# Kernel tuning notes

Hardware: AMD Instinct MI355X
Metric: run time of the kernel (lower is better)

The kernel has to match this reference:

```python
import math
import jax, jax.numpy as jnp
import numpy as np

NH, NKV, HD, THETA = 32, 8, 128, 500000.0

def rotate_half(x):
    x1, x2 = jnp.split(x, 2, axis=-1)
    return jnp.concatenate((-x2, x1), axis=-1)

def rope_cos_sin(seq_len, dim, base, dtype):
    inv_freq = 1.0 / (base ** (jnp.arange(0, dim, 2, dtype=jnp.float32) / dim))
    t = jnp.arange(seq_len, dtype=jnp.float32)
    freqs = jnp.outer(t, inv_freq)              # [S, dim/2]
    emb = jnp.concatenate((freqs, freqs), -1)   # [S, dim]
    return jnp.cos(emb).astype(dtype), jnp.sin(emb).astype(dtype)

def setup_inputs() -> dict:
    key = jax.random.key(0)
    ks = jax.random.split(key, 5)
    B, S, H = 1, 2048, 4096
    sc = 1.0 / math.sqrt(H)
    return {
        'x':  jax.random.normal(ks[0], (B, S, H), jnp.float32),
        'wq': jax.random.normal(ks[1], (H, H), jnp.float32) * sc,
        'wk': jax.random.normal(ks[2], (NKV * HD, H), jnp.float32) * sc,
        'wv': jax.random.normal(ks[3], (NKV * HD, H), jnp.float32) * sc,
        'wo': jax.random.normal(ks[4], (H, H), jnp.float32) * sc,
    }

def attention(x, wq, wk, wv, wo):
    B, S, H = x.shape
    n_rep = NH // NKV
    q = (x @ wq.T).reshape(B, S, NH, HD).transpose(0, 2, 1, 3)    # [B,NH,S,HD]
    k = (x @ wk.T).reshape(B, S, NKV, HD).transpose(0, 2, 1, 3)   # [B,NKV,S,HD]
    v = (x @ wv.T).reshape(B, S, NKV, HD).transpose(0, 2, 1, 3)
    cos, sin = rope_cos_sin(S, HD, THETA, x.dtype)                # [S,HD]
    cos = cos[None, None]; sin = sin[None, None]
    q = q * cos + rotate_half(q) * sin
    k = k * cos + rotate_half(k) * sin
    k = jnp.repeat(k, n_rep, axis=1)                               # [B,NH,S,HD]
    v = jnp.repeat(v, n_rep, axis=1)
    scores = jnp.einsum('bhqd,bhkd->bhqk', q, k) / math.sqrt(HD)
    causal = jnp.tril(jnp.ones((S, S), dtype=bool))
    scores = jnp.where(causal, scores, jnp.finfo(scores.dtype).min)
    probs = jax.nn.softmax(scores, axis=-1)
    out = jnp.einsum('bhqk,bhkd->bhqd', probs, v)                  # [B,NH,S,HD]
    out = out.transpose(0, 2, 1, 3).reshape(B, S, H)
    return out @ wo.T

def reference(x, wq, wk, wv, wo):
    return attention(x, wq, wk, wv, wo)
```

## Files before the change

### kernel.cpp

```cpp
#include <hip/hip_runtime.h>
#include <hip/hip_bf16.h>
#include <math.h>

typedef __bf16 bf16x8 __attribute__((ext_vector_type(8)));
typedef __bf16 bf16x4 __attribute__((ext_vector_type(4)));
typedef unsigned short u16x8 __attribute__((ext_vector_type(8)));
typedef float  f32x4  __attribute__((ext_vector_type(4)));

constexpr int kS   = 2048;
constexpr int kH   = 4096;
constexpr int kNH  = 32;
constexpr int kNKV = 8;
constexpr int kHD  = 128;
constexpr int kQKV = kH + 2 * kNKV * kHD;
constexpr int kKOff = kH;
constexpr int kVOff = kH + kNKV * kHD;

__global__ void cast_bf16(const float* __restrict__ in, __bf16* __restrict__ out, int n4) {
    int i = blockIdx.x * blockDim.x + threadIdx.x;
    if (i < n4) {
        float4 f = ((const float4*)in)[i];
        bf16x4 o;
        o[0] = (__bf16)f.x; o[1] = (__bf16)f.y; o[2] = (__bf16)f.z; o[3] = (__bf16)f.w;
        ((bf16x4*)out)[i] = o;
    }
}

__global__ void cast_all(const float* __restrict__ x, const float* __restrict__ wq,
                         const float* __restrict__ wk, const float* __restrict__ wv,
                         __bf16* __restrict__ xb, __bf16* __restrict__ wqkv) {
    int i = blockIdx.x * 256 + threadIdx.x;
    float4 f;
    __bf16* dst;
    int di;
    if (i < (1 << 21)) {
        f = ((const float4*)x)[i];
        dst = xb; di = i;
    } else {
        int j = i - (1 << 21);
        const float4* s = (j < (1 << 22)) ? ((const float4*)wq + j)
                        : (j < (5 << 20)) ? ((const float4*)wk + (j - (1 << 22)))
                                          : ((const float4*)wv + (j - (5 << 20)));
        f = *s;
        dst = wqkv; di = j;
    }
    bf16x4 o;
    o[0] = (__bf16)f.x; o[1] = (__bf16)f.y; o[2] = (__bf16)f.z; o[3] = (__bf16)f.w;
    ((bf16x4*)dst)[di] = o;
}

__device__ inline void gld16(const __bf16* g, __bf16* l) {
    __builtin_amdgcn_global_load_lds((const __attribute__((address_space(1))) void*)g,
                                     (__attribute__((address_space(3))) void*)l, 16, 0, 0);
}

constexpr int GBK = 32, GBM = 128;

template <typename OutT, int GBN>
__global__ __launch_bounds__(512, 2) void gemm8(const __bf16* __restrict__ A,
                                                const __bf16* __restrict__ B,
                                                OutT* __restrict__ C,
                                                int M, int N, int K, int nbx) {
    constexpr int FM  = 4;
    constexpr int FN  = GBN / 64;
    constexpr int AL  = GBM / 128;
    constexpr int BL  = GBN / 128;
    constexpr int GPK = AL + BL;
    constexpr int ASZ = GBM * GBK;
    constexpr int BSZ = GBN * GBK;

    __shared__ __align__(16) __bf16 Ab[4][ASZ];
    __shared__ __align__(16) __bf16 Bb[4][BSZ];

    const int tid = threadIdx.x, w = tid >> 6, lane = tid & 63;
    const int lr = lane & 15, g = lane >> 4;

    const int nwg = (int)gridDim.x;
    const int bid = (int)blockIdx.x;
    int trow, tcol;
    if (nwg == 256 && nbx == 16) {
        const int xcd = bid & 7, j = bid >> 3;
        trow = (xcd >> 1) * 4 + (j >> 3);
        tcol = (xcd & 1) * 8 + (j & 7);
    } else {
        const int id2 = (bid & 7) * (nwg >> 3) + (bid >> 3);
        trow = id2 / nbx; tcol = id2 % nbx;
    }
    const int m0 = trow * GBM, n0 = tcol * GBN;

    const int wm = (w >> 2) * 64, wn = (w & 3) * (GBN / 4);

    const __bf16* ga[AL]; int la[AL];
    const __bf16* gb[BL]; int lb[BL];
#pragma unroll
    for (int a = 0; a < AL; a++) {
        int G = a * 512 + tid, row = G >> 2;
        int lg = (G & 3) ^ ((row >> 1) & 3);
        ga[a] = A + (size_t)(m0 + row) * K + lg * 8;
        la[a] = G * 8;
    }
#pragma unroll
    for (int b = 0; b < BL; b++) {
        int G = b * 512 + tid, row = G >> 2;
        int lg = (G & 3) ^ ((row >> 1) & 3);
        gb[b] = B + (size_t)(n0 + row) * K + lg * 8;
        lb[b] = G * 8;
    }

    int pao[FM], pbo[FN];
    const int sw = (lr >> 1) & 3;
#pragma unroll
    for (int i = 0; i < FM; i++) pao[i] = (wm + i * 16 + lr) * GBK + ((g ^ sw) * 8);
#pragma unroll
    for (int j = 0; j < FN; j++) pbo[j] = (wn + j * 16 + lr) * GBK + ((g ^ sw) * 8);

    f32x4 acc[FM][FN];
#pragma unroll
    for (int i = 0; i < FM; i++)
#pragma unroll
        for (int j = 0; j < FN; j++) acc[i][j] = (f32x4)(0.f);

    const int NT = K / GBK;

#pragma unroll
    for (int z = 0; z < 3; z++) {
#pragma unroll
        for (int a = 0; a < AL; a++) gld16(ga[a] + z * GBK, &Ab[z][la[a]]);
#pragma unroll
        for (int b = 0; b < BL; b++) gld16(gb[b] + z * GBK, &Bb[z][lb[b]]);
    }
    if constexpr (GPK == 4) asm volatile("s_waitcnt vmcnt(8)" ::: "memory");
    else                    asm volatile("s_waitcnt vmcnt(6)" ::: "memory");
    __builtin_amdgcn_s_barrier();

    for (int Z = 0; Z < NT; ++Z) {
        const int q = Z & 3, qs = (Z + 3) & 3;

        bf16x8 af[FM], bfr[FN];
#pragma unroll
        for (int i = 0; i < FM; i++) af[i]  = *(const bf16x8*)&Ab[q][pao[i]];
#pragma unroll
        for (int j = 0; j < FN; j++) bfr[j] = *(const bf16x8*)&Bb[q][pbo[j]];

        if (Z < NT - 3) {
#pragma unroll
            for (int a = 0; a < AL; a++) gld16(ga[a] + (Z + 3) * GBK, &Ab[qs][la[a]]);
#pragma unroll
            for (int b = 0; b < BL; b++) gld16(gb[b] + (Z + 3) * GBK, &Bb[qs][lb[b]]);
        }

        __builtin_amdgcn_s_barrier();
        __builtin_amdgcn_s_setprio(1);
#pragma unroll
        for (int i = 0; i < FM; i++)
#pragma unroll
            for (int j = 0; j < FN; j++)
                acc[i][j] = __builtin_amdgcn_mfma_f32_16x16x32_bf16(
                    af[i], bfr[j], acc[i][j], 0, 0, 0);
        __builtin_amdgcn_s_setprio(0);

        if (Z < NT - 3) {
            if constexpr (GPK == 4) asm volatile("s_waitcnt vmcnt(8)" ::: "memory");
            else                    asm volatile("s_waitcnt vmcnt(6)" ::: "memory");
        } else if (Z == NT - 3) {
            if constexpr (GPK == 4) asm volatile("s_waitcnt vmcnt(4)" ::: "memory");
            else                    asm volatile("s_waitcnt vmcnt(3)" ::: "memory");
        } else if (Z == NT - 2) {
            asm volatile("s_waitcnt vmcnt(0)" ::: "memory");
        }
        __builtin_amdgcn_s_barrier();
    }

    const int cr = g * 4, cc = lr;
#pragma unroll
    for (int i = 0; i < FM; i++)
#pragma unroll
        for (int j = 0; j < FN; j++) {
            OutT* Cp = C + (size_t)(m0 + wm + i * 16 + cr) * N + (n0 + wn + j * 16 + cc);
#pragma unroll
            for (int r = 0; r < 4; r++) Cp[(size_t)r * N] = (OutT)acc[i][j][r];
        }
}

__global__ void rope_qkv(__bf16* __restrict__ qkv) {
    int idx  = blockIdx.x * 256 + threadIdx.x;
    int d8   = idx & 7;
    int rest = idx >> 3;
    int hh   = rest % (kNH + kNKV);
    int s    = rest / (kNH + kNKV);
    __bf16* base = qkv + (size_t)s * kQKV + ((hh < kNH) ? hh * kHD : kKOff + (hh - kNH) * kHD);
    float sc = (hh < kNH) ? 0.088388347648318447f : 1.0f;
    bf16x8 va = *(const bf16x8*)(base + d8 * 8);
    bf16x8 vb = *(const bf16x8*)(base + 64 + d8 * 8);
    bf16x8 ra, rb;
#pragma unroll
    for (int j = 0; j < 8; j++) {
        int d = d8 * 8 + j;
        float rev = (float)s * exp2f(fmaf((float)d, -0.2958057589f, -2.6514961295f));
        rev -= floorf(rev);
        float ang = rev * 6.28318530718f;
        float sn = __sinf(ang), cs = __cosf(ang);
        float a = (float)va[j], b = (float)vb[j];
        ra[j] = (__bf16)((a * cs - b * sn) * sc);
        rb[j] = (__bf16)((b * cs + a * sn) * sc);
    }
    *(bf16x8*)(base + d8 * 8)      = ra;
    *(bf16x8*)(base + 64 + d8 * 8) = rb;
}

constexpr int VTP = 72;

__global__ __launch_bounds__(256) void flash_attn(const __bf16* __restrict__ qkv,
                                                  __bf16* __restrict__ ob) {
    __shared__ __align__(16) __bf16 Ks[2][64 * 128];
    __shared__ __align__(16) __bf16 Vt[2][128 * VTP];
    __shared__ __align__(16) __bf16 Ps[4 * 16 * 64];

    const int tid  = threadIdx.x;
    const int wave = tid >> 6, lane = tid & 63;
    const int bx   = blockIdx.x;
    const int kvh  = bx & 7;
    const int qt   = 127 - (bx >> 3);
    const int h    = kvh * 4 + wave;
    const int r    = lane & 15, g = lane >> 4;
    const int r7   = r & 7;
    const int qglob = qt * 16 + r;

    __bf16* Pw = Ps + wave * 16 * 64;
    const __bf16* kbase = qkv + kKOff + kvh * kHD;
    const __bf16* vbase = qkv + kVOff + kvh * kHD;

    int krow[4], kgc[4];
#pragma unroll
    for (int c = 0; c < 4; c++) {
        krow[c] = wave * 16 + c * 4 + (lane >> 4);
        kgc[c]  = (lane & 15) ^ (krow[c] & 15);
    }
    int vp[2], vc[2];
#pragma unroll
    for (int i = 0; i < 2; i++) {
        int task = i * 256 + tid;
        vp[i] = task & 31; vc[i] = task >> 5;
    }

    bf16x8 qfrag[4];
    const __bf16* qrow = qkv + (size_t)(qt * 16 + r) * kQKV + h * kHD + g * 8;
#pragma unroll
    for (int c = 0; c < 4; c++) qfrag[c] = *(const bf16x8*)(qrow + c * 32);

    f32x4 o[8];
#pragma unroll
    for (int dt = 0; dt < 8; dt++) o[dt] = (f32x4)(0.f);
    float mrow = -3.0e38f, lrow = 0.f;

    const int nkt = qt / 4 + 1;

    bf16x8 va[2], vb[2];
#pragma unroll
    for (int c = 0; c < 4; c++)
        gld16(kbase + (size_t)krow[c] * kQKV + kgc[c] * 8, &Ks[0][(wave * 4 + c) * 512]);
#pragma unroll
    for (int i = 0; i < 2; i++) {
        const __bf16* v0 = vbase + (size_t)(2 * vp[i]) * kQKV + vc[i] * 8;
        va[i] = *(const bf16x8*)v0;
        vb[i] = *(const bf16x8*)(v0 + kQKV);
    }
    asm volatile("s_waitcnt vmcnt(0)" ::: "memory");
#pragma unroll
    for (int i = 0; i < 2; i++) {
        u16x8 a = __builtin_bit_cast(u16x8, va[i]);
        u16x8 b = __builtin_bit_cast(u16x8, vb[i]);
#pragma unroll
        for (int j = 0; j < 8; j++) {
            unsigned int pk = (unsigned int)a[j] | ((unsigned int)b[j] << 16);
            *(unsigned int*)(&Vt[0][(vc[i] * 8 + j) * VTP + 2 * vp[i]]) = pk;
        }
    }
    __syncthreads();

    for (int kt = 0; kt < nkt; ++kt) {
        const int cur = kt & 1, nb = cur ^ 1;
        const bool nxt = (kt + 1) < nkt;

        if (nxt) {
#pragma unroll
            for (int c = 0; c < 4; c++)
                gld16(kbase + (size_t)((kt + 1) * 64 + krow[c]) * kQKV + kgc[c] * 8,
                      &Ks[nb][(wave * 4 + c) * 512]);
#pragma unroll
            for (int i = 0; i < 2; i++) {
                const __bf16* v0 = vbase + (size_t)((kt + 1) * 64 + 2 * vp[i]) * kQKV + vc[i] * 8;
                va[i] = *(const bf16x8*)v0;
                vb[i] = *(const bf16x8*)(v0 + kQKV);
            }
        }

        f32x4 st[4];
#pragma unroll
        for (int t = 0; t < 4; t++) st[t] = (f32x4)(0.f);
#pragma unroll
        for (int c = 0; c < 4; c++) {
#pragma unroll
            for (int t = 0; t < 4; t++) {
                bf16x8 kf = *(const bf16x8*)&Ks[cur][(t * 16 + r) * 128 + (((c * 4 + g) ^ r) * 8)];
                st[t] = __builtin_amdgcn_mfma_f32_16x16x32_bf16(kf, qfrag[c], st[t], 0, 0, 0);
            }
        }

        if (kt == nkt - 1) {
#pragma unroll
            for (int t = 0; t < 4; t++)
#pragma unroll
                for (int reg = 0; reg < 4; reg++) {
                    int key = kt * 64 + t * 16 + g * 4 + reg;
                    if (key > qglob) st[t][reg] = -3.0e38f;
                }
        }

        float mloc = -3.0e38f;
#pragma unroll
        for (int t = 0; t < 4; t++)
#pragma unroll
            for (int reg = 0; reg < 4; reg++) mloc = fmaxf(mloc, st[t][reg]);
        mloc = fmaxf(mloc, __shfl_xor(mloc, 16));
        mloc = fmaxf(mloc, __shfl_xor(mloc, 32));
        float mnew  = fmaxf(mrow, mloc);
        float alpha = __expf(mrow - mnew);
        mrow = mnew;
        float lsum = 0.f;
#pragma unroll
        for (int t = 0; t < 4; t++)
#pragma unroll
            for (int reg = 0; reg < 4; reg++) {
                float pv = __expf(st[t][reg] - mnew);
                st[t][reg] = pv;
                lsum += pv;
            }
        lsum += __shfl_xor(lsum, 16);
        lsum += __shfl_xor(lsum, 32);
        lrow = lrow * alpha + lsum;

        float ar[4];
#pragma unroll
        for (int reg = 0; reg < 4; reg++) ar[reg] = __shfl(alpha, g * 4 + reg);
#pragma unroll
        for (int dt = 0; dt < 8; dt++)
#pragma unroll
            for (int reg = 0; reg < 4; reg++) o[dt][reg] *= ar[reg];

        if (nxt) {
            asm volatile("s_waitcnt vmcnt(0)" ::: "memory");
#pragma unroll
            for (int i = 0; i < 2; i++) {
                u16x8 a = __builtin_bit_cast(u16x8, va[i]);
                u16x8 b = __builtin_bit_cast(u16x8, vb[i]);
#pragma unroll
                for (int j = 0; j < 8; j++) {
                    unsigned int pk = (unsigned int)a[j] | ((unsigned int)b[j] << 16);
                    *(unsigned int*)(&Vt[nb][(vc[i] * 8 + j) * VTP + 2 * vp[i]]) = pk;
                }
            }
        }

#pragma unroll
        for (int t = 0; t < 4; t++) {
            bf16x4 pb;
#pragma unroll
            for (int j = 0; j < 4; j++) pb[j] = (__bf16)st[t][j];
            int p8 = t * 4 + g;
            *(bf16x4*)&Pw[r * 64 + (((p8 >> 1) ^ r7) * 8) + ((p8 & 1) * 4)] = pb;
        }
        __asm__ volatile("s_waitcnt lgkmcnt(0)" ::: "memory");

#pragma unroll
        for (int kc = 0; kc < 2; kc++) {
            bf16x8 pf = *(const bf16x8*)&Pw[r * 64 + (((kc * 4 + g) ^ r7) * 8)];
#pragma unroll
            for (int dt = 0; dt < 8; dt++) {
                bf16x8 vf = *(const bf16x8*)&Vt[cur][(dt * 16 + r) * VTP + kc * 32 + g * 8];
                o[dt] = __builtin_amdgcn_mfma_f32_16x16x32_bf16(pf, vf, o[dt], 0, 0, 0);
            }
        }
        __syncthreads();
    }

    float linv = 1.f / lrow;
    float lr4[4];
#pragma unroll
    for (int reg = 0; reg < 4; reg++) lr4[reg] = __shfl(linv, g * 4 + reg);
#pragma unroll
    for (int dt = 0; dt < 8; dt++)
#pragma unroll
        for (int reg = 0; reg < 4; reg++) {
            int qq = g * 4 + reg, dd = dt * 16 + r;
            ob[(size_t)(qt * 16 + qq) * kH + h * kHD + dd] = (__bf16)(o[dt][reg] * lr4[reg]);
        }
}

extern "C" void kernel_launch(void* const* d_in, const int* in_sizes, int n_in,
                              void* d_out, int out_size, void* d_ws, size_t ws_size,
                              hipStream_t stream) {
    const float* x  = (const float*)d_in[0];
    const float* wq = (const float*)d_in[1];
    const float* wk = (const float*)d_in[2];
    const float* wv = (const float*)d_in[3];
    const float* wo = (const float*)d_in[4];
    float* out = (float*)d_out;

    char* p = (char*)d_ws;
    auto alloc = [&](size_t bytes) {
        char* r = p;
        p += (bytes + 255) & ~(size_t)255;
        return r;
    };
    __bf16* xb    = (__bf16*)alloc((size_t)kS * kH * 2);
    __bf16* wqkvb = (__bf16*)alloc((size_t)kQKV * kH * 2);
    __bf16* qkv   = (__bf16*)alloc((size_t)kS * kQKV * 2);
    __bf16* ao    = xb;
    __bf16* wob   = wqkvb;

    cast_all<<<dim3(1 << 15), 256, 0, stream>>>(x, wq, wk, wv, xb, wqkvb);

    gemm8<__bf16, 384><<<dim3((kS / GBM) * (kQKV / 384)), 512, 0, stream>>>(
        xb, wqkvb, qkv, kS, kQKV, kH, kQKV / 384);

    rope_qkv<<<dim3(kS * (kNH + kNKV) * 8 / 256), 256, 0, stream>>>(qkv);

    cast_bf16<<<dim3((kH * kH / 4) / 256), 256, 0, stream>>>(wo, wob, kH * kH / 4);

    flash_attn<<<dim3(kNKV * (kS / 16)), 256, 0, stream>>>(qkv, ao);

    gemm8<float, 256><<<dim3((kS / GBM) * (kH / 256)), 512, 0, stream>>>(
        ao, wob, out, kS, kH, kH, kH / 256);
}
```

Before: 472.1 us.

## Add 256x256 ping-pong GEMM for QKV projection and fuse wo cast

Replaces the QKV projection GEMM with a new 256x256-tile kernel. It double-buffers LDS with a 64-wide K step and splits each K step into four quadrant phases, interleaving async global-to-LDS loads with MFMA work and raising wave priority around the MFMA blocks. The wo fp32-to-bf16 cast moves into the single cast_all launch, which drops one kernel launch and now needs a separate wob buffer instead of reusing wqkvb. Priority hints are also added around the MFMA loops in flash attention. The larger tiles raise register and LDS pressure, and the grid has only 192 workgroups, which may underfill the GPU.

```diff
diff --git a/kernel.cpp b/kernel.cpp
--- a/kernel.cpp
+++ b/kernel.cpp
@@ -16,19 +16,11 @@
 constexpr int kKOff = kH;
 constexpr int kVOff = kH + kNKV * kHD;
 
-__global__ void cast_bf16(const float* __restrict__ in, __bf16* __restrict__ out, int n4) {
-    int i = blockIdx.x * blockDim.x + threadIdx.x;
-    if (i < n4) {
-        float4 f = ((const float4*)in)[i];
-        bf16x4 o;
-        o[0] = (__bf16)f.x; o[1] = (__bf16)f.y; o[2] = (__bf16)f.z; o[3] = (__bf16)f.w;
-        ((bf16x4*)out)[i] = o;
-    }
-}
-
 __global__ void cast_all(const float* __restrict__ x, const float* __restrict__ wq,
                          const float* __restrict__ wk, const float* __restrict__ wv,
-                         __bf16* __restrict__ xb, __bf16* __restrict__ wqkv) {
+                         const float* __restrict__ wo,
+                         __bf16* __restrict__ xb, __bf16* __restrict__ wqkv,
+                         __bf16* __restrict__ wob) {
     int i = blockIdx.x * 256 + threadIdx.x;
     float4 f;
     __bf16* dst;
@@ -38,11 +30,17 @@
         dst = xb; di = i;
     } else {
         int j = i - (1 << 21);
-        const float4* s = (j < (1 << 22)) ? ((const float4*)wq + j)
-                        : (j < (5 << 20)) ? ((const float4*)wk + (j - (1 << 22)))
-                                          : ((const float4*)wv + (j - (5 << 20)));
-        f = *s;
-        dst = wqkv; di = j;
+        if (j < (6 << 20)) {
+            const float4* s = (j < (1 << 22)) ? ((const float4*)wq + j)
+                            : (j < (5 << 20)) ? ((const float4*)wk + (j - (1 << 22)))
+                                              : ((const float4*)wv + (j - (5 << 20)));
+            f = *s;
+            dst = wqkv; di = j;
+        } else {
+            int k = j - (6 << 20);
+            f = ((const float4*)wo)[k];
+            dst = wob; di = k;
+        }
     }
     bf16x4 o;
     o[0] = (__bf16)f.x; o[1] = (__bf16)f.y; o[2] = (__bf16)f.z; o[3] = (__bf16)f.w;
@@ -52,6 +50,122 @@
 __device__ inline void gld16(const __bf16* g, __bf16* l) {
     __builtin_amdgcn_global_load_lds((const __attribute__((address_space(1))) void*)g,
                                      (__attribute__((address_space(3))) void*)l, 16, 0, 0);
+}
+
+constexpr int TBK = 64;
+
+__global__ __launch_bounds__(512, 2) void gemm256(const __bf16* __restrict__ A,
+                                                  const __bf16* __restrict__ B,
+                                                  __bf16* __restrict__ C,
+                                                  int M, int N, int K, int nbx) {
+    __shared__ __align__(16) __bf16 Ab[2][256 * TBK];
+    __shared__ __align__(16) __bf16 Bb[2][256 * TBK];
+
+    const int tid = threadIdx.x, w = tid >> 6, lane = tid & 63;
+    const int lr = lane & 15, g4 = lane >> 4, s7 = lane & 7;
+
+    const int nwg = (int)gridDim.x, bid = (int)blockIdx.x;
+    const int id2 = (bid & 7) * (nwg >> 3) + (bid >> 3);
+    const int m0 = (id2 / nbx) * 256, n0 = (id2 % nbx) * 256;
+
+    const int wmq = (w >> 2) * 64;
+    const int wnq = (w & 3) * 32;
+
+    const int srow = tid >> 3;
+    const int slg  = (tid & 7) ^ (srow & 7);
+    const __bf16* gA = A + (size_t)(m0 + srow) * K + slg * 8;
+    const __bf16* gB = B + (size_t)(n0 + srow) * K + slg * 8;
+
+    int pk[2];
+#pragma unroll
+    for (int kc = 0; kc < 2; kc++) pk[kc] = (((kc * 4 + g4) ^ s7) * 8);
+
+    bf16x8 a[4][2], b[2][2];
+    f32x4 acc[8][4];
+#pragma unroll
+    for (int i = 0; i < 8; i++)
+#pragma unroll
+        for (int j = 0; j < 4; j++) acc[i][j] = (f32x4)(0.f);
+
+    const int NT = K / TBK;
+
+#define STAGE_A(h, kt, bf) { _Pragma("unroll") for (int e = 0; e < 2; e++) \
+    gld16(gA + (size_t)((h) * 128 + e * 64) * K + (kt) * TBK, \
+          &Ab[bf][(h) * 8192 + (e * 512 + tid) * 8]); }
+#define STAGE_B(h, kt, bf) { _Pragma("unroll") for (int e = 0; e < 2; e++) \
+    gld16(gB + (size_t)((h) * 128 + e * 64) * K + (kt) * TBK, \
+          &Bb[bf][(h) * 8192 + (e * 512 + tid) * 8]); }
+#define DSA(qi) { _Pragma("unroll") for (int i = 0; i < 4; i++) { \
+    const int ro = ((qi) * 128 + wmq + i * 16 + lr) * TBK; \
+    a[i][0] = *(const bf16x8*)&Ab[q][ro + pk[0]]; \
+    a[i][1] = *(const bf16x8*)&Ab[q][ro + pk[1]]; } }
+#define DSB(qj) { _Pragma("unroll") for (int j = 0; j < 2; j++) { \
+    const int ro = ((qj) * 128 + wnq + j * 16 + lr) * TBK; \
+    b[j][0] = *(const bf16x8*)&Bb[q][ro + pk[0]]; \
+    b[j][1] = *(const bf16x8*)&Bb[q][ro + pk[1]]; } }
+#define MMA(qi, qj) { _Pragma("unroll") for (int kc = 0; kc < 2; kc++) \
+    _Pragma("unroll") for (int i = 0; i < 4; i++) \
+    _Pragma("unroll") for (int j = 0; j < 2; j++) \
+        acc[(qi) * 4 + i][(qj) * 2 + j] = __builtin_amdgcn_mfma_f32_16x16x32_bf16( \
+            a[i][kc], b[j][kc], acc[(qi) * 4 + i][(qj) * 2 + j], 0, 0, 0); }
+#define LGKM0 asm volatile("s_waitcnt lgkmcnt(0)" ::: "memory")
+#define VM(n) asm volatile("s_waitcnt vmcnt(" #n ")" ::: "memory")
+#define BAR __builtin_amdgcn_s_barrier()
+#define PRIO(x) __builtin_amdgcn_s_setprio(x)
+
+    STAGE_A(0, 0, 0); STAGE_B(0, 0, 0); STAGE_A(1, 0, 0); STAGE_B(1, 0, 0);
+    VM(4);
+    BAR;
+
+    for (int Z = 0; Z < NT; ++Z) {
+        const int q = Z & 1, nb = q ^ 1;
+        const bool stg = Z < NT - 1;
+
+        DSA(0); DSB(0);
+        if (stg) STAGE_A(0, Z + 1, nb);
+        BAR; LGKM0;
+        PRIO(1); MMA(0, 0); PRIO(0);
+        if (stg) { VM(4); } else { VM(2); }
+        BAR;
+
+        DSA(1);
+        if (stg) STAGE_B(0, Z + 1, nb);
+        BAR; LGKM0;
+        PRIO(1); MMA(1, 0); PRIO(0);
+        if (stg) { VM(4); } else { VM(0); }
+        BAR;
+
+        DSB(1);
+        if (stg) STAGE_A(1, Z + 1, nb);
+        BAR; LGKM0;
+        PRIO(1); MMA(1, 1); PRIO(0);
+        BAR;
+
+        DSA(0);
+        if (stg) STAGE_B(1, Z + 1, nb);
+        BAR; LGKM0;
+        PRIO(1); MMA(0, 1); PRIO(0);
+        if (stg) { VM(4); }
+        BAR;
+    }
+
+#undef STAGE_A
+#undef STAGE_B
+#undef DSA
+#undef DSB
+#undef MMA
+
+    const int cr = g4 * 4, cc = lr;
+#pragma unroll
+    for (int fi = 0; fi < 8; fi++)
+#pragma unroll
+        for (int fj = 0; fj < 4; fj++) {
+            const int row = m0 + (fi >> 2) * 128 + wmq + (fi & 3) * 16 + cr;
+            const int col = n0 + (fj >> 1) * 128 + wnq + (fj & 1) * 16 + cc;
+            __bf16* Cp = C + (size_t)row * N + col;
+#pragma unroll
+            for (int r = 0; r < 4; r++) Cp[(size_t)r * N] = (__bf16)acc[fi][fj][r];
+        }
 }
 
 constexpr int GBK = 32, GBM = 128;
@@ -298,6 +412,7 @@
         f32x4 st[4];
 #pragma unroll
         for (int t = 0; t < 4; t++) st[t] = (f32x4)(0.f);
+        __builtin_amdgcn_s_setprio(1);
 #pragma unroll
         for (int c = 0; c < 4; c++) {
 #pragma unroll
@@ -306,6 +421,7 @@
                 st[t] = __builtin_amdgcn_mfma_f32_16x16x32_bf16(kf, qfrag[c], st[t], 0, 0, 0);
             }
         }
+        __builtin_amdgcn_s_setprio(0);
 
         if (kt == nkt - 1) {
 #pragma unroll
@@ -372,6 +488,7 @@
         }
         __asm__ volatile("s_waitcnt lgkmcnt(0)" ::: "memory");
 
+        __builtin_amdgcn_s_setprio(1);
 #pragma unroll
         for (int kc = 0; kc < 2; kc++) {
             bf16x8 pf = *(const bf16x8*)&Pw[r * 64 + (((kc * 4 + g) ^ r7) * 8)];
@@ -381,6 +498,7 @@
                 o[dt] = __builtin_amdgcn_mfma_f32_16x16x32_bf16(pf, vf, o[dt], 0, 0, 0);
             }
         }
+        __builtin_amdgcn_s_setprio(0);
         __syncthreads();
     }
 
@@ -416,17 +534,15 @@
     __bf16* xb    = (__bf16*)alloc((size_t)kS * kH * 2);
     __bf16* wqkvb = (__bf16*)alloc((size_t)kQKV * kH * 2);
     __bf16* qkv   = (__bf16*)alloc((size_t)kS * kQKV * 2);
+    __bf16* wob   = (__bf16*)alloc((size_t)kH * kH * 2);
     __bf16* ao    = xb;
-    __bf16* wob   = wqkvb;
-
-    cast_all<<<dim3(1 << 15), 256, 0, stream>>>(x, wq, wk, wv, xb, wqkvb);
-
-    gemm8<__bf16, 384><<<dim3((kS / GBM) * (kQKV / 384)), 512, 0, stream>>>(
-        xb, wqkvb, qkv, kS, kQKV, kH, kQKV / 384);
+
+    cast_all<<<dim3(49152), 256, 0, stream>>>(x, wq, wk, wv, wo, xb, wqkvb, wob);
+
+    gemm256<<<dim3((kS / 256) * (kQKV / 256)), 512, 0, stream>>>(
+        xb, wqkvb, qkv, kS, kQKV, kH, kQKV / 256);
 
     rope_qkv<<<dim3(kS * (kNH + kNKV) * 8 / 256), 256, 0, stream>>>(qkv);
-
-    cast_bf16<<<dim3((kH * kH / 4) / 256), 256, 0, stream>>>(wo, wob, kH * kH / 4);
 
     flash_attn<<<dim3(kNKV * (kS / 16)), 256, 0, stream>>>(qkv, ao);
 
```

Result: slower. 522.2 us (+10.6%).

## Process two query tiles per wave in flash attention and fold wo cast into cast_all

Applied to the files above, without the earlier changes.

Each flash-attention wave now handles two 16-row query fragments (32 queries per block), so every K/V tile loaded into LDS feeds twice as many MFMAs and the grid is halved. The K/V double buffering is removed in favour of single-buffered loads with a synchronous wait, with launch_bounds(256,2) and s_setprio raised around the MFMA sections. Query tiles are ordered to interleave long and short causal rows for balance. The wo weight cast is merged into the single cast_all launch with its own workspace buffer, dropping a separate kernel launch. The cost is that load latency is no longer overlapped within a block and more registers are used.

```diff
diff --git a/kernel.cpp b/kernel.cpp
--- a/kernel.cpp
+++ b/kernel.cpp
@@ -16,19 +16,11 @@
 constexpr int kKOff = kH;
 constexpr int kVOff = kH + kNKV * kHD;
 
-__global__ void cast_bf16(const float* __restrict__ in, __bf16* __restrict__ out, int n4) {
-    int i = blockIdx.x * blockDim.x + threadIdx.x;
-    if (i < n4) {
-        float4 f = ((const float4*)in)[i];
-        bf16x4 o;
-        o[0] = (__bf16)f.x; o[1] = (__bf16)f.y; o[2] = (__bf16)f.z; o[3] = (__bf16)f.w;
-        ((bf16x4*)out)[i] = o;
-    }
-}
-
 __global__ void cast_all(const float* __restrict__ x, const float* __restrict__ wq,
                          const float* __restrict__ wk, const float* __restrict__ wv,
-                         __bf16* __restrict__ xb, __bf16* __restrict__ wqkv) {
+                         const float* __restrict__ wo,
+                         __bf16* __restrict__ xb, __bf16* __restrict__ wqkv,
+                         __bf16* __restrict__ wob) {
     int i = blockIdx.x * 256 + threadIdx.x;
     float4 f;
     __bf16* dst;
@@ -38,11 +30,17 @@
         dst = xb; di = i;
     } else {
         int j = i - (1 << 21);
-        const float4* s = (j < (1 << 22)) ? ((const float4*)wq + j)
-                        : (j < (5 << 20)) ? ((const float4*)wk + (j - (1 << 22)))
-                                          : ((const float4*)wv + (j - (5 << 20)));
-        f = *s;
-        dst = wqkv; di = j;
+        if (j < (6 << 20)) {
+            const float4* s = (j < (1 << 22)) ? ((const float4*)wq + j)
+                            : (j < (5 << 20)) ? ((const float4*)wk + (j - (1 << 22)))
+                                              : ((const float4*)wv + (j - (5 << 20)));
+            f = *s;
+            dst = wqkv; di = j;
+        } else {
+            int k = j - (6 << 20);
+            f = ((const float4*)wo)[k];
+            dst = wob; di = k;
+        }
     }
     bf16x4 o;
     o[0] = (__bf16)f.x; o[1] = (__bf16)f.y; o[2] = (__bf16)f.z; o[3] = (__bf16)f.w;
@@ -210,23 +208,22 @@
 
 constexpr int VTP = 72;
 
-__global__ __launch_bounds__(256) void flash_attn(const __bf16* __restrict__ qkv,
-                                                  __bf16* __restrict__ ob) {
-    __shared__ __align__(16) __bf16 Ks[2][64 * 128];
-    __shared__ __align__(16) __bf16 Vt[2][128 * VTP];
-    __shared__ __align__(16) __bf16 Ps[4 * 16 * 64];
+__global__ __launch_bounds__(256, 2) void flash_attn(const __bf16* __restrict__ qkv,
+                                                     __bf16* __restrict__ ob) {
+    __shared__ __align__(16) __bf16 Ks[64 * 128];
+    __shared__ __align__(16) __bf16 Vt[128 * VTP];
+    __shared__ __align__(16) __bf16 Ps[8 * 16 * 64];
 
     const int tid  = threadIdx.x;
     const int wave = tid >> 6, lane = tid & 63;
     const int bx   = blockIdx.x;
     const int kvh  = bx & 7;
-    const int qt   = 127 - (bx >> 3);
+    const int p    = bx >> 3;
+    const int qt2  = (p < 32) ? (63 - p) : (p - 32);
     const int h    = kvh * 4 + wave;
     const int r    = lane & 15, g = lane >> 4;
     const int r7   = r & 7;
-    const int qglob = qt * 16 + r;
-
-    __bf16* Pw = Ps + wave * 16 * 64;
+
     const __bf16* kbase = qkv + kKOff + kvh * kHD;
     const __bf16* vbase = qkv + kVOff + kvh * kHD;
 
@@ -243,158 +240,154 @@
         vp[i] = task & 31; vc[i] = task >> 5;
     }
 
-    bf16x8 qfrag[4];
-    const __bf16* qrow = qkv + (size_t)(qt * 16 + r) * kQKV + h * kHD + g * 8;
-#pragma unroll
-    for (int c = 0; c < 4; c++) qfrag[c] = *(const bf16x8*)(qrow + c * 32);
-
-    f32x4 o[8];
-#pragma unroll
-    for (int dt = 0; dt < 8; dt++) o[dt] = (f32x4)(0.f);
-    float mrow = -3.0e38f, lrow = 0.f;
-
-    const int nkt = qt / 4 + 1;
-
-    bf16x8 va[2], vb[2];
-#pragma unroll
-    for (int c = 0; c < 4; c++)
-        gld16(kbase + (size_t)krow[c] * kQKV + kgc[c] * 8, &Ks[0][(wave * 4 + c) * 512]);
-#pragma unroll
-    for (int i = 0; i < 2; i++) {
-        const __bf16* v0 = vbase + (size_t)(2 * vp[i]) * kQKV + vc[i] * 8;
-        va[i] = *(const bf16x8*)v0;
-        vb[i] = *(const bf16x8*)(v0 + kQKV);
-    }
-    asm volatile("s_waitcnt vmcnt(0)" ::: "memory");
-#pragma unroll
-    for (int i = 0; i < 2; i++) {
-        u16x8 a = __builtin_bit_cast(u16x8, va[i]);
-        u16x8 b = __builtin_bit_cast(u16x8, vb[i]);
-#pragma unroll
-        for (int j = 0; j < 8; j++) {
-            unsigned int pk = (unsigned int)a[j] | ((unsigned int)b[j] << 16);
-            *(unsigned int*)(&Vt[0][(vc[i] * 8 + j) * VTP + 2 * vp[i]]) = pk;
-        }
-    }
-    __syncthreads();
-
+    bf16x8 qfrag[2][4];
+#pragma unroll
+    for (int f = 0; f < 2; f++) {
+        const __bf16* qrow = qkv + (size_t)(qt2 * 32 + f * 16 + r) * kQKV + h * kHD + g * 8;
+#pragma unroll
+        for (int c = 0; c < 4; c++) qfrag[f][c] = *(const bf16x8*)(qrow + c * 32);
+    }
+
+    f32x4 o[2][8];
+#pragma unroll
+    for (int f = 0; f < 2; f++)
+#pragma unroll
+        for (int dt = 0; dt < 8; dt++) o[f][dt] = (f32x4)(0.f);
+    float mrow[2] = {-3.0e38f, -3.0e38f}, lrow[2] = {0.f, 0.f};
+
+    const int nkt = qt2 / 2 + 1;
     for (int kt = 0; kt < nkt; ++kt) {
-        const int cur = kt & 1, nb = cur ^ 1;
-        const bool nxt = (kt + 1) < nkt;
-
-        if (nxt) {
-#pragma unroll
-            for (int c = 0; c < 4; c++)
-                gld16(kbase + (size_t)((kt + 1) * 64 + krow[c]) * kQKV + kgc[c] * 8,
-                      &Ks[nb][(wave * 4 + c) * 512]);
-#pragma unroll
-            for (int i = 0; i < 2; i++) {
-                const __bf16* v0 = vbase + (size_t)((kt + 1) * 64 + 2 * vp[i]) * kQKV + vc[i] * 8;
-                va[i] = *(const bf16x8*)v0;
-                vb[i] = *(const bf16x8*)(v0 + kQKV);
-            }
-        }
-
-        f32x4 st[4];
-#pragma unroll
-        for (int t = 0; t < 4; t++) st[t] = (f32x4)(0.f);
+#pragma unroll
+        for (int c = 0; c < 4; c++)
+            gld16(kbase + (size_t)(kt * 64 + krow[c]) * kQKV + kgc[c] * 8,
+                  Ks + (wave * 4 + c) * 512);
+        bf16x8 va[2], vb[2];
+#pragma unroll
+        for (int i = 0; i < 2; i++) {
+            const __bf16* v0 = vbase + (size_t)(kt * 64 + 2 * vp[i]) * kQKV + vc[i] * 8;
+            va[i] = *(const bf16x8*)v0;
+            vb[i] = *(const bf16x8*)(v0 + kQKV);
+        }
+        asm volatile("s_waitcnt vmcnt(0)" ::: "memory");
+#pragma unroll
+        for (int i = 0; i < 2; i++) {
+            u16x8 a = __builtin_bit_cast(u16x8, va[i]);
+            u16x8 b = __builtin_bit_cast(u16x8, vb[i]);
+#pragma unroll
+            for (int j = 0; j < 8; j++) {
+                unsigned int pk = (unsigned int)a[j] | ((unsigned int)b[j] << 16);
+                *(unsigned int*)(&Vt[(vc[i] * 8 + j) * VTP + 2 * vp[i]]) = pk;
+            }
+        }
+        __syncthreads();
+
+        f32x4 st[2][4];
+#pragma unroll
+        for (int f = 0; f < 2; f++)
+#pragma unroll
+            for (int t = 0; t < 4; t++) st[f][t] = (f32x4)(0.f);
+        __builtin_amdgcn_s_setprio(1);
 #pragma unroll
         for (int c = 0; c < 4; c++) {
 #pragma unroll
             for (int t = 0; t < 4; t++) {
-                bf16x8 kf = *(const bf16x8*)&Ks[cur][(t * 16 + r) * 128 + (((c * 4 + g) ^ r) * 8)];
-                st[t] = __builtin_amdgcn_mfma_f32_16x16x32_bf16(kf, qfrag[c], st[t], 0, 0, 0);
-            }
-        }
+                bf16x8 kf = *(const bf16x8*)&Ks[(t * 16 + r) * 128 + (((c * 4 + g) ^ r) * 8)];
+                st[0][t] = __builtin_amdgcn_mfma_f32_16x16x32_bf16(kf, qfrag[0][c], st[0][t], 0, 0, 0);
+                st[1][t] = __builtin_amdgcn_mfma_f32_16x16x32_bf16(kf, qfrag[1][c], st[1][t], 0, 0, 0);
+            }
+        }
+        __builtin_amdgcn_s_setprio(0);
 
         if (kt == nkt - 1) {
 #pragma unroll
+            for (int f = 0; f < 2; f++) {
+                const int qg = qt2 * 32 + f * 16 + r;
+#pragma unroll
+                for (int t = 0; t < 4; t++)
+#pragma unroll
+                    for (int reg = 0; reg < 4; reg++) {
+                        int key = kt * 64 + t * 16 + g * 4 + reg;
+                        if (key > qg) st[f][t][reg] = -3.0e38f;
+                    }
+            }
+        }
+
+#pragma unroll
+        for (int f = 0; f < 2; f++) {
+            float mloc = -3.0e38f;
+#pragma unroll
             for (int t = 0; t < 4; t++)
 #pragma unroll
+                for (int reg = 0; reg < 4; reg++) mloc = fmaxf(mloc, st[f][t][reg]);
+            mloc = fmaxf(mloc, __shfl_xor(mloc, 16));
+            mloc = fmaxf(mloc, __shfl_xor(mloc, 32));
+            float mnew  = fmaxf(mrow[f], mloc);
+            float alpha = __expf(mrow[f] - mnew);
+            mrow[f] = mnew;
+            float lsum = 0.f;
+#pragma unroll
+            for (int t = 0; t < 4; t++)
+#pragma unroll
                 for (int reg = 0; reg < 4; reg++) {
-                    int key = kt * 64 + t * 16 + g * 4 + reg;
-                    if (key > qglob) st[t][reg] = -3.0e38f;
+                    float pv = __expf(st[f][t][reg] - mnew);
+                    st[f][t][reg] = pv;
+                    lsum += pv;
                 }
-        }
-
-        float mloc = -3.0e38f;
-#pragma unroll
-        for (int t = 0; t < 4; t++)
-#pragma unroll
-            for (int reg = 0; reg < 4; reg++) mloc = fmaxf(mloc, st[t][reg]);
-        mloc = fmaxf(mloc, __shfl_xor(mloc, 16));
-        mloc = fmaxf(mloc, __shfl_xor(mloc, 32));
-        float mnew  = fmaxf(mrow, mloc);
-        float alpha = __expf(mrow - mnew);
-        mrow = mnew;
-        float lsum = 0.f;
-#pragma unroll
-        for (int t = 0; t < 4; t++)
+            lsum += __shfl_xor(lsum, 16);
+            lsum += __shfl_xor(lsum, 32);
+            lrow[f] = lrow[f] * alpha + lsum;
+
+            float ar[4];
+#pragma unroll
+            for (int reg = 0; reg < 4; reg++) ar[reg] = __shfl(alpha, g * 4 + reg);
+#pragma unroll
+            for (int dt = 0; dt < 8; dt++)
+#pragma unroll
+                for (int reg = 0; reg < 4; reg++) o[f][dt][reg] *= ar[reg];
+
+            __bf16* Pw = Ps + (wave * 2 + f) * 1024;
+#pragma unroll
+            for (int t = 0; t < 4; t++) {
+                bf16x4 pb;
+#pragma unroll
+                for (int j = 0; j < 4; j++) pb[j] = (__bf16)st[f][t][j];
+                int p8 = t * 4 + g;
+                *(bf16x4*)&Pw[r * 64 + (((p8 >> 1) ^ r7) * 8) + ((p8 & 1) * 4)] = pb;
+            }
+        }
+        __asm__ volatile("s_waitcnt lgkmcnt(0)" ::: "memory");
+
+        __builtin_amdgcn_s_setprio(1);
+#pragma unroll
+        for (int kc = 0; kc < 2; kc++) {
+            bf16x8 pf0 = *(const bf16x8*)&Ps[(wave * 2 + 0) * 1024 + r * 64 + (((kc * 4 + g) ^ r7) * 8)];
+            bf16x8 pf1 = *(const bf16x8*)&Ps[(wave * 2 + 1) * 1024 + r * 64 + (((kc * 4 + g) ^ r7) * 8)];
+#pragma unroll
+            for (int dt = 0; dt < 8; dt++) {
+                bf16x8 vf = *(const bf16x8*)&Vt[(dt * 16 + r) * VTP + kc * 32 + g * 8];
+                o[0][dt] = __builtin_amdgcn_mfma_f32_16x16x32_bf16(pf0, vf, o[0][dt], 0, 0, 0);
+                o[1][dt] = __builtin_amdgcn_mfma_f32_16x16x32_bf16(pf1, vf, o[1][dt], 0, 0, 0);
+            }
+        }
+        __builtin_amdgcn_s_setprio(0);
+        __syncthreads();
+    }
+
+#pragma unroll
+    for (int f = 0; f < 2; f++) {
+        float linv = 1.f / lrow[f];
+        float lr4[4];
+#pragma unroll
+        for (int reg = 0; reg < 4; reg++) lr4[reg] = __shfl(linv, g * 4 + reg);
+#pragma unroll
+        for (int dt = 0; dt < 8; dt++)
 #pragma unroll
             for (int reg = 0; reg < 4; reg++) {
-                float pv = __expf(st[t][reg] - mnew);
-                st[t][reg] = pv;
-                lsum += pv;
-            }
-        lsum += __shfl_xor(lsum, 16);
-        lsum += __shfl_xor(lsum, 32);
-        lrow = lrow * alpha + lsum;
-
-        float ar[4];
-#pragma unroll
-        for (int reg = 0; reg < 4; reg++) ar[reg] = __shfl(alpha, g * 4 + reg);
-#pragma unroll
-        for (int dt = 0; dt < 8; dt++)
-#pragma unroll
-            for (int reg = 0; reg < 4; reg++) o[dt][reg] *= ar[reg];
-
-        if (nxt) {
-            asm volatile("s_waitcnt vmcnt(0)" ::: "memory");
-#pragma unroll
-            for (int i = 0; i < 2; i++) {
-                u16x8 a = __builtin_bit_cast(u16x8, va[i]);
-                u16x8 b = __builtin_bit_cast(u16x8, vb[i]);
-#pragma unroll
-                for (int j = 0; j < 8; j++) {
-                    unsigned int pk = (unsigned int)a[j] | ((unsigned int)b[j] << 16);
-                    *(unsigned int*)(&Vt[nb][(vc[i] * 8 + j) * VTP + 2 * vp[i]]) = pk;
-                }
-            }
-        }
-
-#pragma unroll
-        for (int t = 0; t < 4; t++) {
-            bf16x4 pb;
-#pragma unroll
-            for (int j = 0; j < 4; j++) pb[j] = (__bf16)st[t][j];
-            int p8 = t * 4 + g;
-            *(bf16x4*)&Pw[r * 64 + (((p8 >> 1) ^ r7) * 8) + ((p8 & 1) * 4)] = pb;
-        }
-        __asm__ volatile("s_waitcnt lgkmcnt(0)" ::: "memory");
-
-#pragma unroll
-        for (int kc = 0; kc < 2; kc++) {
-            bf16x8 pf = *(const bf16x8*)&Pw[r * 64 + (((kc * 4 + g) ^ r7) * 8)];
-#pragma unroll
-            for (int dt = 0; dt < 8; dt++) {
-                bf16x8 vf = *(const bf16x8*)&Vt[cur][(dt * 16 + r) * VTP + kc * 32 + g * 8];
-                o[dt] = __builtin_amdgcn_mfma_f32_16x16x32_bf16(pf, vf, o[dt], 0, 0, 0);
-            }
-        }
-        __syncthreads();
-    }
-
-    float linv = 1.f / lrow;
-    float lr4[4];
-#pragma unroll
-    for (int reg = 0; reg < 4; reg++) lr4[reg] = __shfl(linv, g * 4 + reg);
-#pragma unroll
-    for (int dt = 0; dt < 8; dt++)
-#pragma unroll
-        for (int reg = 0; reg < 4; reg++) {
-            int qq = g * 4 + reg, dd = dt * 16 + r;
-            ob[(size_t)(qt * 16 + qq) * kH + h * kHD + dd] = (__bf16)(o[dt][reg] * lr4[reg]);
-        }
+                int qq = g * 4 + reg, dd = dt * 16 + r;
+                ob[(size_t)(qt2 * 32 + f * 16 + qq) * kH + h * kHD + dd]
+                    = (__bf16)(o[f][dt][reg] * lr4[reg]);
+            }
+    }
 }
 
 extern "C" void kernel_launch(void* const* d_in, const int* in_sizes, int n_in,
@@ -416,19 +409,17 @@
     __bf16* xb    = (__bf16*)alloc((size_t)kS * kH * 2);
     __bf16* wqkvb = (__bf16*)alloc((size_t)kQKV * kH * 2);
     __bf16* qkv   = (__bf16*)alloc((size_t)kS * kQKV * 2);
+    __bf16* wob   = (__bf16*)alloc((size_t)kH * kH * 2);
     __bf16* ao    = xb;
-    __bf16* wob   = wqkvb;
-
-    cast_all<<<dim3(1 << 15), 256, 0, stream>>>(x, wq, wk, wv, xb, wqkvb);
+
+    cast_all<<<dim3(49152), 256, 0, stream>>>(x, wq, wk, wv, wo, xb, wqkvb, wob);
 
     gemm8<__bf16, 384><<<dim3((kS / GBM) * (kQKV / 384)), 512, 0, stream>>>(
         xb, wqkvb, qkv, kS, kQKV, kH, kQKV / 384);
 
     rope_qkv<<<dim3(kS * (kNH + kNKV) * 8 / 256), 256, 0, stream>>>(qkv);
 
-    cast_bf16<<<dim3((kH * kH / 4) / 256), 256, 0, stream>>>(wo, wob, kH * kH / 4);
-
-    flash_attn<<<dim3(kNKV * (kS / 16)), 256, 0, stream>>>(qkv, ao);
+    flash_attn<<<dim3(kNKV * (kS / 32)), 256, 0, stream>>>(qkv, ao);
 
     gemm8<float, 256><<<dim3((kS / GBM) * (kH / 256)), 512, 0, stream>>>(
         ao, wob, out, kS, kH, kH, kH / 256);
```

Measured after the change: 488.9 us. 3.6% more time.
